# Kernel optimization log

Hardware: AMD Instinct MI355X
Metric: run time of the kernel (lower is better)

The kernel has to match this reference:

```python
import jax, jax.numpy as jnp
import numpy as np

MIN_HAIRPIN = 4
BIG = 1e30  # stand-in for the numpy reference's 1e18 INF (fp32-safe)


def _dp_single(e_pair, e_unp, allowed):
    """Nussinov min-energy DP for one sequence.
    e_pair: (L,L) f32, e_unp: (L,) f32, allowed: (L,L) bool.
    Returns dp (L,L) and ptr (L,L) backpointers matching the numpy reference:
      0 -> i unpaired, 1 -> j unpaired, 2 -> (i,j) paired, k+3 -> bifurcation at k.
    Vectorised over the antidiagonal (all i for a fixed span s at once).
    """
    L = e_unp.shape[0]
    idx = jnp.arange(L)
    dp0 = jnp.full((L, L), BIG, dtype=e_pair.dtype).at[idx, idx].set(e_unp)
    ptr0 = jnp.full((L, L), -1, dtype=jnp.int32).at[idx, idx].set(0)
    t = jnp.arange(L - 1)  # bifurcation offset k = i + t

    def step(carry, s):
        dp, ptr = carry
        j = idx + s - 1
        valid = j < L
        jc = jnp.minimum(j, L - 1)
        ip1 = jnp.minimum(idx + 1, L - 1)
        jm1 = jnp.maximum(jc - 1, 0)
        opt0 = dp[ip1, jc] + e_unp            # i unpaired
        opt1 = dp[idx, jm1] + e_unp[jc]       # j unpaired
        inner = jnp.where(s >= 3, dp[ip1, jm1], 0.0)
        pair_ok = allowed[idx, jc] & (s - 1 > MIN_HAIRPIN)  # j - i = s - 1
        opt2 = jnp.where(pair_ok, inner + e_pair[idx, jc], BIG)
        k = jnp.minimum(idx[:, None] + t[None, :], L - 1)
        bif = dp[idx[:, None], k] + dp[jnp.minimum(k + 1, L - 1), jc[:, None]]
        bif = jnp.where(t[None, :] < s - 1, bif, BIG)
        cand = jnp.concatenate([opt0[:, None], opt1[:, None], opt2[:, None], bif], axis=1)
        c = jnp.argmin(cand, axis=1)  # first-occurrence argmin == strict-< tie-break
        best = jnp.take_along_axis(cand, c[:, None], axis=1)[:, 0]
        new_ptr = jnp.where(c < 3, c, c + idx).astype(jnp.int32)  # c-3 is offset t -> k+3 = c+i
        dp = dp.at[idx, jc].set(jnp.where(valid, best, dp[idx, jc]))
        ptr = ptr.at[idx, jc].set(jnp.where(valid, new_ptr, ptr[idx, jc]))
        return (dp, ptr), None

    (dp, ptr), _ = jax.lax.scan(step, (dp0, ptr0), jnp.arange(2, L + 1))
    return dp, ptr


def _traceback(ptr):
    """Stack-based traceback of the backpointer matrix. Returns pairs (L,) int32, -1 = unpaired."""
    L = ptr.shape[0]

    def cond(st):
        return st[2] > 0

    def body(st):
        si, sj, sp, res = st
        top = sp - 1
        i, j = si[top], sj[top]
        skip = i >= j
        p = ptr[i, j]
        is0, is1, is2, isk = p == 0, p == 1, p == 2, p >= 3
        k = p - 3
        p1i = jnp.where(is0 | is2, i + 1, i)
        p1j = jnp.where(is1 | is2, j - 1, jnp.where(isk, k, j))
        v1 = (~skip) & jnp.where(is2, i + 1 <= j - 1, True)
        v2 = (~skip) & isk  # bifurcation pushes a second interval (k+1, j)
        res = jnp.where(is2 & (~skip), res.at[i].set(j).at[j].set(i), res)
        si = si.at[top].set(jnp.where(v1, p1i, si[top]))
        sj = sj.at[top].set(jnp.where(v1, p1j, sj[top]))
        slot2 = top + v1.astype(jnp.int32)
        si = si.at[slot2].set(jnp.where(v2, k + 1, si[slot2]))
        sj = sj.at[slot2].set(jnp.where(v2, j, sj[slot2]))
        sp = top + v1.astype(jnp.int32) + v2.astype(jnp.int32)
        return si, sj, sp, res

    si0 = jnp.zeros((L,), jnp.int32)
    sj0 = jnp.zeros((L,), jnp.int32).at[0].set(L - 1)
    res0 = jnp.full((L,), -1, jnp.int32)
    _, _, _, res = jax.lax.while_loop(cond, body, (si0, sj0, jnp.int32(1), res0))
    return res


def _structure_energy(e_pair, e_unp, pairs):
    """E(x,S) = sum_{i unpaired} e_unp[i] + sum_{(i,j) in S, i<j} e_pair[i,j]."""
    L = e_unp.shape[-1]
    clamped = jnp.maximum(pairs, 0)
    unp = jnp.where(pairs < 0, e_unp, 0.0).sum(-1)
    pe = jnp.take_along_axis(e_pair, clamped[..., None], axis=2)[..., 0]
    is_pair = (pairs >= 0) & (jnp.arange(L)[None, :] < clamped)
    return unp + jnp.where(is_pair, pe, 0.0).sum(-1)


def setup_inputs() -> dict:
    key = jax.random.key(0)
    k1, k2, k3 = jax.random.split(key, 3)
    B, L = 32, 384
    e_pair = jax.random.normal(k1, (B, L, L), jnp.float32)
    e_unp = jax.random.normal(k2, (B, L), jnp.float32)
    pair_mask = jax.random.randint(k3, (B, L, L), 0, 2).astype(jnp.bool_)
    return {"e_pair": e_pair, "e_unp": e_unp, "pair_mask": pair_mask}


def reference(e_pair, e_unp, pair_mask):
    dp, ptr = jax.vmap(_dp_single)(e_pair, e_unp, pair_mask)
    pairs = jax.vmap(_traceback)(ptr)  # (B, L) int32, -1 = unpaired
    energy = _structure_energy(e_pair, e_unp, pairs)  # (B,), equals dp[:, 0, -1]
    return pairs, energy
```

## Files before the change

### kernel.cpp

```cpp
#include <hip/hip_runtime.h>
#include <hip/hip_bf16.h>

#define LSEQ 384
#define BATCH 32
#define BIGV 1e30f
#define TB_STK 448
#define NN ((size_t)LSEQ * LSEQ)
#define BT 32
#define NT 12
#define PIT 33

__device__ __forceinline__ int detect_mmode_wave(const unsigned char* m0, int lane) {
    unsigned char v = m0[lane & 63];
    unsigned long long big = __ballot(v >= 2);
    unsigned long long off = __ballot((((lane & 63) & 3) != 0) && (v != 0));
    return big ? 2 : (off ? 1 : 0);
}
__device__ __forceinline__ bool mask_read(const void* mask, size_t idx, int mmode) {
    if (mmode == 0) return ((const unsigned int*)mask)[idx] != 0;
    if (mmode == 1) return ((const unsigned char*)mask)[idx] != 0;
    return ((const unsigned short*)mask)[idx] != 0;
}
__device__ __forceinline__ void choice_write(void* mask, size_t idx, int c, int mmode) {
    if (mmode == 0) ((unsigned int*)mask)[idx] = (unsigned int)c;
    else if (mmode == 1) ((unsigned char*)mask)[idx] = (unsigned char)c;
    else ((unsigned short*)mask)[idx] = (unsigned short)c;
}

__device__ __forceinline__ float edge_min32(const float* rowp, const float* colp) {
    float a0 = BIGV, a1 = BIGV, a2 = BIGV, a3 = BIGV;
    #pragma unroll
    for (int kk = 0; kk < 32; kk += 4) {
        float r0 = rowp[kk], r1 = rowp[kk + 1], r2 = rowp[kk + 2], r3 = rowp[kk + 3];
        const float* cb = colp + kk * PIT;
        float c0 = cb[0], c1 = cb[PIT], c2 = cb[2 * PIT], c3 = cb[3 * PIT];
        a0 = fminf(a0, r0 + c0); a1 = fminf(a1, r1 + c1);
        a2 = fminf(a2, r2 + c2); a3 = fminf(a3, r3 + c3);
    }
    return fminf(fminf(a0, a1), fminf(a2, a3));
}

__global__ __launch_bounds__(64) void diag_kernel(
    float* __restrict__ e_pair, const float* __restrict__ e_unp, void* mask)
{
    __shared__ float dT[BT + 1][PIT];
    __shared__ float epm[BT][PIT];
    __shared__ float s_eunp[BT];

    const int bid = blockIdx.x;
    const int b = bid / NT, t = bid % NT;
    const int lane = threadIdx.x;
    float* dpG = e_pair + (size_t)b * NN;
    const size_t mb = (size_t)b * NN;
    const int mmode = detect_mmode_wave((const unsigned char*)mask, lane);

    for (int z = lane; z < (BT + 1) * PIT; z += 64) ((float*)dT)[z] = BIGV;
    __syncthreads();
    if (lane < BT) {
        int i = t * BT + lane;
        float v = e_unp[b * LSEQ + i];
        s_eunp[lane] = v;
        dT[lane][lane] = v;
        dpG[(size_t)i * LSEQ + i] = v;
        if (i > 0) dpG[(size_t)i * LSEQ + i - 1] = v;
    }
    for (int z = lane; z < BT * BT; z += 64) {
        int li = z >> 5, lj = z & 31;
        int i = t * BT + li, j = t * BT + lj;
        bool ok = (lj - li > 4) && mask_read(mask, mb + (size_t)i * LSEQ + j, mmode);
        epm[li][lj] = ok ? dpG[(size_t)i * LSEQ + j] : BIGV;
    }
    __syncthreads();

    const int idx = lane >> 1, h = lane & 1;
    for (int sg = 1; sg < BT; ++sg) {
        const int nc = BT - sg;
        const bool act = idx < nc;
        const int li = idx, lj = idx + sg;
        const int ljc = lj < BT ? lj : BT - 1;
        const int i = t * BT + li, j = t * BT + lj;
        float ev = edge_min32(&dT[li][0], &dT[1][ljc]);
        float e1 = BIGV, opt0 = 0.f, x1 = BIGV, x2 = BIGV;
        if (act) {
            if (h == 0) {
                e1 = ev;
                opt0 = dT[li + 1][lj] + s_eunp[li];
            } else {
                x1 = dT[li][lj - 1] + s_eunp[lj];
                float pe = epm[li][lj];
                if (pe < BIGV) x2 = dT[li + 1][lj - 1] + pe;
            }
        }
        float y1 = __shfl_xor(x1, 1), y2 = __shfl_xor(x2, 1);
        if (act && h == 0) {
            float best = fminf(e1, y2);
            int cch = (best == opt0) ? 0 : (best == y1) ? 1
                     : (best == y2 && y2 < BIGV) ? 2 : 3;
            dT[li][lj] = best;
            dpG[(size_t)i * LSEQ + j] = best;
            if (i > 0) dpG[(size_t)j * LSEQ + i - 1] = best;
            choice_write(mask, mb + (size_t)j * LSEQ + i, cch, mmode);
        }
    }
}

__global__ __launch_bounds__(512) void phase_kernel(
    float* __restrict__ e_pair, const float* __restrict__ e_unp, void* mask, int s)
{
    __shared__ float dTI[BT + 1][PIT], dTJ[BT + 1][PIT];
    __shared__ float cur[BT + 1][PIT];
    __shared__ float epm[BT][PIT];
    __shared__ float part[8][BT][PIT];
    __shared__ float brow[BT], bcol[BT], s_eI[BT], s_eJ[BT];
    __shared__ float bcorn;

    const int nt = NT - s;
    const int bid = blockIdx.x;
    const int b = bid / nt, I = bid % nt, J = I + s;
    const int tid = threadIdx.x, lane = tid & 63, wv = tid >> 6;
    float* dpG = e_pair + (size_t)b * NN;
    const size_t mb = (size_t)b * NN;
    const int mmode = detect_mmode_wave((const unsigned char*)mask, lane);

    for (int z = tid; z < BT * BT; z += 512) {
        int li = z >> 5, lj = z & 31;
        dTI[li][lj] = (lj >= li) ? dpG[(size_t)(I * BT + li) * LSEQ + I * BT + lj] : BIGV;
        dTJ[li][lj] = (lj >= li) ? dpG[(size_t)(J * BT + li) * LSEQ + J * BT + lj] : BIGV;
    }
    for (int z = tid; z < PIT; z += 512) {
        dTI[BT][z] = BIGV; dTJ[BT][z] = BIGV; cur[BT][z] = BIGV;
    }
    if (tid < BT) {
        brow[tid] = dpG[(size_t)((I + 1) * BT) * LSEQ + J * BT + tid];
        s_eI[tid] = e_unp[b * LSEQ + I * BT + tid];
    } else if (tid < 2 * BT) {
        int q = tid - BT;
        bcol[q] = dpG[(size_t)(I * BT + q) * LSEQ + J * BT - 1];
        s_eJ[q] = e_unp[b * LSEQ + J * BT + q];
    } else if (tid == 2 * BT) {
        bcorn = (s >= 2) ? dpG[(size_t)((I + 1) * BT) * LSEQ + J * BT - 1] : BIGV;
    }
    for (int z = tid; z < BT * BT; z += 512) {
        int li = z >> 5, lj = z & 31;
        int i = I * BT + li, j = J * BT + lj;
        bool ok = (j - i > 4) && mask_read(mask, mb + (size_t)i * LSEQ + j, mmode);
        epm[li][lj] = ok ? dpG[(size_t)i * LSEQ + j] : BIGV;
    }

    if (s == 1) {
        for (int z = tid; z < BT * PIT; z += 512) ((float*)cur)[z] = BIGV;
    } else {
        const int r0 = (lane >> 3) << 2, c0 = (lane & 7) << 2;
        float r16[16];
        #pragma unroll
        for (int z = 0; z < 16; ++z) r16[z] = BIGV;
        for (int M = I + 1 + wv; M < J; M += 8) {
            #pragma unroll
            for (int kq = 0; kq < 8; ++kq) {
                const int k = M * BT + kq * 4;
                float4 a0 = *(const float4*)&dpG[(size_t)(I * BT + r0 + 0) * LSEQ + k];
                float4 a1 = *(const float4*)&dpG[(size_t)(I * BT + r0 + 1) * LSEQ + k];
                float4 a2 = *(const float4*)&dpG[(size_t)(I * BT + r0 + 2) * LSEQ + k];
                float4 a3 = *(const float4*)&dpG[(size_t)(I * BT + r0 + 3) * LSEQ + k];
                float4 b0 = *(const float4*)&dpG[(size_t)(J * BT + c0 + 0) * LSEQ + k];
                float4 b1 = *(const float4*)&dpG[(size_t)(J * BT + c0 + 1) * LSEQ + k];
                float4 b2 = *(const float4*)&dpG[(size_t)(J * BT + c0 + 2) * LSEQ + k];
                float4 b3 = *(const float4*)&dpG[(size_t)(J * BT + c0 + 3) * LSEQ + k];
                #pragma unroll
                for (int ri = 0; ri < 4; ++ri) {
                    float4 av = ri == 0 ? a0 : ri == 1 ? a1 : ri == 2 ? a2 : a3;
                    #pragma unroll
                    for (int ci = 0; ci < 4; ++ci) {
                        float4 bv = ci == 0 ? b0 : ci == 1 ? b1 : ci == 2 ? b2 : b3;
                        float m = fminf(fminf(av.x + bv.x, av.y + bv.y),
                                        fminf(av.z + bv.z, av.w + bv.w));
                        r16[ri * 4 + ci] = fminf(r16[ri * 4 + ci], m);
                    }
                }
            }
        }
        #pragma unroll
        for (int ri = 0; ri < 4; ++ri)
            #pragma unroll
            for (int ci = 0; ci < 4; ++ci)
                part[wv][r0 + ri][c0 + ci] = r16[ri * 4 + ci];
        __syncthreads();
        for (int z = tid; z < BT * BT; z += 512) {
            int li = z >> 5, lj = z & 31;
            float m01 = fminf(part[0][li][lj], part[1][li][lj]);
            float m23 = fminf(part[2][li][lj], part[3][li][lj]);
            float m45 = fminf(part[4][li][lj], part[5][li][lj]);
            float m67 = fminf(part[6][li][lj], part[7][li][lj]);
            cur[li][lj] = fminf(fminf(m01, m23), fminf(m45, m67));
        }
    }
    __syncthreads();
    if (wv != 0) return;

    const int idx = lane >> 1, h = lane & 1;
    for (int sg = -(BT - 1); sg <= BT - 1; ++sg) {
        const int asg = sg < 0 ? -sg : sg;
        const int nc = BT - asg;
        const bool act = idx < nc;
        const int li = (sg >= 0) ? idx : idx - sg;
        const int lj = li + sg;
        const int lic = li < BT ? li : BT - 1;
        const int ljc = (lj < BT ? (lj >= 0 ? lj : 0) : BT - 1);
        const int i = I * BT + li, j = J * BT + lj;
        const float* rowp = (h == 0) ? &dTI[lic][0] : &cur[lic][0];
        const float* colp = (h == 0) ? &cur[1][ljc] : &dTJ[1][ljc];
        float ev = edge_min32(rowp, colp);
        float e1 = BIGV, opt0 = 0.f, farv = BIGV;
        float x0 = BIGV, x1 = BIGV, x2 = BIGV;
        if (act) {
            if (h == 0) {
                e1 = fminf(ev, dTI[li][BT - 1] + brow[lj]);
                opt0 = ((li + 1 < BT) ? cur[li + 1][lj] : brow[lj]) + s_eI[li];
                farv = cur[li][lj];
            } else {
                x0 = ev;
                x1 = ((lj >= 1) ? cur[li][lj - 1] : bcol[li]) + s_eJ[lj];
                float pe = epm[li][lj];
                if (pe < BIGV) {
                    float inner = (li + 1 < BT)
                        ? ((lj >= 1) ? cur[li + 1][lj - 1] : bcol[li + 1])
                        : ((lj >= 1) ? brow[lj - 1] : bcorn);
                    x2 = inner + pe;
                }
            }
        }
        float y0 = __shfl_xor(x0, 1), y1 = __shfl_xor(x1, 1), y2 = __shfl_xor(x2, 1);
        if (act && h == 0) {
            float best = fminf(fminf(fminf(e1, y0), farv), y2);
            int cch = (best == opt0) ? 0 : (best == y1) ? 1
                     : (best == y2 && y2 < BIGV) ? 2 : 3;
            cur[li][lj] = best;
            dpG[(size_t)i * LSEQ + j] = best;
            if (i > 0) dpG[(size_t)j * LSEQ + i - 1] = best;
            choice_write(mask, mb + (size_t)j * LSEQ + i, cch, mmode);
        }
    }
}

__global__ __launch_bounds__(512) void tb_kernel(
    const float* __restrict__ e_pair, const void* mask, float* __restrict__ out)
{
    const int b = blockIdx.x;
    const int tid = threadIdx.x;
    const int lane = tid & 63, wv = tid >> 6;
    const float* dp = e_pair + (size_t)b * NN;
    const size_t mb = (size_t)b * NN;
    const int mmode = detect_mmode_wave((const unsigned char*)mask, lane);

    __shared__ __align__(16) unsigned char ch[LSEQ * LSEQ];
    __shared__ short res[LSEQ];
    __shared__ int st[TB_STK];

    if (mmode == 1) {
        const uint4* src = (const uint4*)((const unsigned char*)mask + mb);
        for (int z = tid; z < (int)(NN / 16); z += 512) ((uint4*)ch)[z] = src[z];
    } else if (mmode == 2) {
        const uint4* src = (const uint4*)((const unsigned char*)mask + mb * 2);
        for (int z = tid; z < (int)(NN / 8); z += 512) {
            uint4 v = src[z];
            unsigned int lo = (v.x & 0xFFu) | (((v.x >> 16) & 0xFFu) << 8)
                            | ((v.y & 0xFFu) << 16) | (((v.y >> 16) & 0xFFu) << 24);
            unsigned int hi = (v.z & 0xFFu) | (((v.z >> 16) & 0xFFu) << 8)
                            | ((v.w & 0xFFu) << 16) | (((v.w >> 16) & 0xFFu) << 24);
            ((unsigned int*)ch)[z * 2] = lo;
            ((unsigned int*)ch)[z * 2 + 1] = hi;
        }
    } else {
        const uint4* src = (const uint4*)((const unsigned char*)mask + mb * 4);
        for (int z = tid; z < (int)(NN / 4); z += 512) {
            uint4 v = src[z];
            ((unsigned int*)ch)[z] = (v.x & 0xFFu) | ((v.y & 0xFFu) << 8)
                                   | ((v.z & 0xFFu) << 16) | ((v.w & 0xFFu) << 24);
        }
    }
    for (int l = tid; l < LSEQ; l += 512) res[l] = -1;
    __syncthreads();
    if (wv != 0) return;

    int sp = 0;
    int ci = 0, cj = LSEQ - 1;
    int have = 1;
    for (int iter = 0; iter < 8192; ++iter) {
        if (!have) {
            if (sp == 0) break;
            --sp;
            int pk = st[sp];
            ci = pk >> 16; cj = pk & 0xFFFF;
        }
        have = 0;
        if (ci >= cj) continue;
        int c = ch[(size_t)cj * LSEQ + ci];
        if (c == 0) { ++ci; have = 1; }
        else if (c == 1) { --cj; have = 1; }
        else if (c == 2) {
            res[ci] = (short)cj; res[cj] = (short)ci;
            if (ci + 1 <= cj - 1) { ++ci; --cj; have = 1; }
        } else {
            const int d = cj - ci;
            const float* rowi = dp + (size_t)ci * LSEQ;
            const float* mrow = dp + (size_t)cj * LSEQ;
            float bv = BIGV; int bt = d;
            for (int t = lane; t < d; t += 64) {
                float cc = rowi[ci + t] + mrow[ci + t];
                if (cc < bv || (cc == bv && t < bt)) { bv = cc; bt = t; }
            }
            for (int m = 32; m > 0; m >>= 1) {
                float ov = __shfl_xor(bv, m, 64);
                int   ot = __shfl_xor(bt, m, 64);
                if (ov < bv || (ov == bv && ot < bt)) { bv = ov; bt = ot; }
            }
            int k = ci + bt;
            if (sp < TB_STK - 1) { st[sp] = ((k + 1) << 16) | cj; ++sp; }
            cj = k; have = 1;
        }
    }

    for (int l = lane; l < LSEQ; l += 64)
        out[b * LSEQ + l] = (float)res[l];
    if (lane == 0)
        out[BATCH * LSEQ + b] = dp[LSEQ - 1];
}

extern "C" void kernel_launch(void* const* d_in, const int* in_sizes, int n_in,
                              void* d_out, int out_size, void* d_ws, size_t ws_size,
                              hipStream_t stream) {
    float* e_pair = (float*)d_in[0];
    const float* e_unp = (const float*)d_in[1];
    void* mask = d_in[2];
    (void)d_ws; (void)ws_size;

    diag_kernel<<<BATCH * NT, 64, 0, stream>>>(e_pair, e_unp, mask);
    for (int s = 1; s < NT; ++s)
        phase_kernel<<<BATCH * (NT - s), 512, 0, stream>>>(e_pair, e_unp, mask, s);
    tb_kernel<<<BATCH, 512, 0, stream>>>(e_pair, mask, (float*)d_out);
}
```

Baseline: 912.0 us.

## Fuse per-span DP phases into one persistent row-wise kernel with atomic counters

Replaces the diagonal kernel and the eleven per-span phase launches with a single persistent kernel. Each workgroup grabs a tile-row job from an atomic queue and walks its spans in order, waiting on per-batch span counters in global memory instead of kernel boundaries. Previously computed tiles of the same row stay in shared memory and are reused for the bifurcation min-plus step, so only the column tiles are read from global memory. The change trades launch overhead and redundant row reloads for spin-wait synchronisation, relaxed atomic loads and stores, and fewer waves per block (256 threads instead of 512). Correctness depends on relaxed ordering plus vmcnt waits and a capped spin loop.

```diff
diff --git a/kernel.cpp b/kernel.cpp
--- a/kernel.cpp
+++ b/kernel.cpp
@@ -1,5 +1,4 @@
 #include <hip/hip_runtime.h>
-#include <hip/hip_bf16.h>
 
 #define LSEQ 384
 #define BATCH 32
@@ -9,6 +8,9 @@
 #define BT 32
 #define NT 12
 #define PIT 33
+#define NJOBS (BATCH * NT)
+#define WS_CNT_BASE 8
+#define SPIN_CAP (1 << 21)
 
 __device__ __forceinline__ int detect_mmode_wave(const unsigned char* m0, int lane) {
     unsigned char v = m0[lane & 63];
@@ -21,10 +23,29 @@
     if (mmode == 1) return ((const unsigned char*)mask)[idx] != 0;
     return ((const unsigned short*)mask)[idx] != 0;
 }
-__device__ __forceinline__ void choice_write(void* mask, size_t idx, int c, int mmode) {
-    if (mmode == 0) ((unsigned int*)mask)[idx] = (unsigned int)c;
-    else if (mmode == 1) ((unsigned char*)mask)[idx] = (unsigned char)c;
-    else ((unsigned short*)mask)[idx] = (unsigned short)c;
+__device__ __forceinline__ void choice_write_rel(void* mask, size_t idx, int c, int mmode) {
+    if (mmode == 0)
+        __hip_atomic_store((unsigned int*)mask + idx, (unsigned int)c,
+                           __ATOMIC_RELAXED, __HIP_MEMORY_SCOPE_AGENT);
+    else if (mmode == 1)
+        __hip_atomic_store((unsigned char*)mask + idx, (unsigned char)c,
+                           __ATOMIC_RELAXED, __HIP_MEMORY_SCOPE_AGENT);
+    else
+        __hip_atomic_store((unsigned short*)mask + idx, (unsigned short)c,
+                           __ATOMIC_RELAXED, __HIP_MEMORY_SCOPE_AGENT);
+}
+__device__ __forceinline__ float aload(const float* p) {
+    return __hip_atomic_load((float*)p, __ATOMIC_RELAXED, __HIP_MEMORY_SCOPE_AGENT);
+}
+__device__ __forceinline__ float4 aload4(const float* p) {
+    union { unsigned long long u[2]; float4 f; } r;
+    unsigned long long* q = (unsigned long long*)p;
+    r.u[0] = __hip_atomic_load(q, __ATOMIC_RELAXED, __HIP_MEMORY_SCOPE_AGENT);
+    r.u[1] = __hip_atomic_load(q + 1, __ATOMIC_RELAXED, __HIP_MEMORY_SCOPE_AGENT);
+    return r.f;
+}
+__device__ __forceinline__ void astore(float* p, float v) {
+    __hip_atomic_store(p, v, __ATOMIC_RELAXED, __HIP_MEMORY_SCOPE_AGENT);
 }
 
 __device__ __forceinline__ float edge_min32(const float* rowp, const float* colp) {
@@ -40,204 +61,227 @@
     return fminf(fminf(a0, a1), fminf(a2, a3));
 }
 
-__global__ __launch_bounds__(64) void diag_kernel(
-    float* __restrict__ e_pair, const float* __restrict__ e_unp, void* mask)
+__global__ void init_ws(unsigned int* __restrict__ ws) {
+    for (int z = threadIdx.x; z < WS_CNT_BASE + BATCH * 16; z += 256) ws[z] = 0;
+}
+
+__global__ __launch_bounds__(256) void dp_rows(
+    float* __restrict__ e_pair, const float* __restrict__ e_unp,
+    void* mask, unsigned int* __restrict__ ws)
 {
-    __shared__ float dT[BT + 1][PIT];
+    __shared__ float rowT[NT][BT + 1][PIT];
+    __shared__ float dTJ[BT + 1][PIT];
     __shared__ float epm[BT][PIT];
-    __shared__ float s_eunp[BT];
-
-    const int bid = blockIdx.x;
-    const int b = bid / NT, t = bid % NT;
-    const int lane = threadIdx.x;
-    float* dpG = e_pair + (size_t)b * NN;
-    const size_t mb = (size_t)b * NN;
+    __shared__ float brow[BT], s_eI[BT], s_eJ[BT];
+    __shared__ float bcorn_s;
+    __shared__ unsigned int s_job;
+
+    const int tid = threadIdx.x, lane = tid & 63, wv = tid >> 6;
     const int mmode = detect_mmode_wave((const unsigned char*)mask, lane);
 
-    for (int z = lane; z < (BT + 1) * PIT; z += 64) ((float*)dT)[z] = BIGV;
-    __syncthreads();
-    if (lane < BT) {
-        int i = t * BT + lane;
-        float v = e_unp[b * LSEQ + i];
-        s_eunp[lane] = v;
-        dT[lane][lane] = v;
-        dpG[(size_t)i * LSEQ + i] = v;
-        if (i > 0) dpG[(size_t)i * LSEQ + i - 1] = v;
-    }
-    for (int z = lane; z < BT * BT; z += 64) {
-        int li = z >> 5, lj = z & 31;
-        int i = t * BT + li, j = t * BT + lj;
-        bool ok = (lj - li > 4) && mask_read(mask, mb + (size_t)i * LSEQ + j, mmode);
-        epm[li][lj] = ok ? dpG[(size_t)i * LSEQ + j] : BIGV;
-    }
-    __syncthreads();
-
-    const int idx = lane >> 1, h = lane & 1;
-    for (int sg = 1; sg < BT; ++sg) {
-        const int nc = BT - sg;
-        const bool act = idx < nc;
-        const int li = idx, lj = idx + sg;
-        const int ljc = lj < BT ? lj : BT - 1;
-        const int i = t * BT + li, j = t * BT + lj;
-        float ev = edge_min32(&dT[li][0], &dT[1][ljc]);
-        float e1 = BIGV, opt0 = 0.f, x1 = BIGV, x2 = BIGV;
-        if (act) {
-            if (h == 0) {
-                e1 = ev;
-                opt0 = dT[li + 1][lj] + s_eunp[li];
+    for (;;) {
+        if (tid == 0)
+            s_job = __hip_atomic_fetch_add(&ws[0], 1u, __ATOMIC_RELAXED,
+                                           __HIP_MEMORY_SCOPE_AGENT);
+        __syncthreads();
+        const unsigned int job = s_job;
+        if (job >= NJOBS) return;
+        const int b = (int)(job / NT);
+        const int I = (int)(job % NT);
+        float* dpG = e_pair + (size_t)b * NN;
+        const size_t mb = (size_t)b * NN;
+        unsigned int* cnt = ws + WS_CNT_BASE + b * 16;
+
+        for (int z = tid; z < NT * (BT + 1) * PIT; z += 256) ((float*)rowT)[z] = BIGV;
+        for (int z = tid; z < (BT + 1) * PIT; z += 256) ((float*)dTJ)[z] = BIGV;
+        if (tid < BT) s_eI[tid] = e_unp[b * LSEQ + I * BT + tid];
+        __syncthreads();
+
+        if (tid < BT) {
+            int i = I * BT + tid;
+            float v = s_eI[tid];
+            rowT[0][tid][tid] = v;
+            astore(&dpG[(size_t)i * LSEQ + i], v);
+            if (i > 0) astore(&dpG[(size_t)i * LSEQ + i - 1], v);
+        }
+        for (int z = tid; z < BT * BT; z += 256) {
+            int li = z >> 5, lj = z & 31;
+            int i = I * BT + li, j = I * BT + lj;
+            bool ok = (lj - li > 4) && mask_read(mask, mb + (size_t)i * LSEQ + j, mmode);
+            epm[li][lj] = ok ? dpG[(size_t)i * LSEQ + j] : BIGV;
+        }
+        __syncthreads();
+        if (wv == 0) {
+            const int idx = lane >> 1, h = lane & 1;
+            for (int sg = 1; sg < BT; ++sg) {
+                const int nc = BT - sg;
+                const bool act = idx < nc;
+                const int li = idx, lj = idx + sg;
+                const int ljc = lj < BT ? lj : BT - 1;
+                const int i = I * BT + li, j = I * BT + lj;
+                float ev = edge_min32(&rowT[0][li][0], &rowT[0][1][ljc]);
+                float e1 = BIGV, opt0 = 0.f, x1 = BIGV, x2 = BIGV;
+                if (act) {
+                    if (h == 0) {
+                        e1 = ev;
+                        opt0 = rowT[0][li + 1][lj] + s_eI[li];
+                    } else {
+                        x1 = rowT[0][li][lj - 1] + s_eI[lj];
+                        float pe = epm[li][lj];
+                        if (pe < BIGV) x2 = rowT[0][li + 1][lj - 1] + pe;
+                    }
+                }
+                float y1 = __shfl_xor(x1, 1), y2 = __shfl_xor(x2, 1);
+                if (act && h == 0) {
+                    float best = fminf(e1, y2);
+                    int cch = (best == opt0) ? 0 : (best == y1) ? 1
+                             : (best == y2 && y2 < BIGV) ? 2 : 3;
+                    rowT[0][li][lj] = best;
+                    astore(&dpG[(size_t)i * LSEQ + j], best);
+                    if (i > 0) astore(&dpG[(size_t)j * LSEQ + i - 1], best);
+                    choice_write_rel(mask, mb + (size_t)j * LSEQ + i, cch, mmode);
+                }
+            }
+        }
+        asm volatile("s_waitcnt vmcnt(0)" ::: "memory");
+        __syncthreads();
+        if (tid == 0)
+            __hip_atomic_fetch_add(&cnt[0], 1u, __ATOMIC_RELAXED,
+                                   __HIP_MEMORY_SCOPE_AGENT);
+
+        for (int s = 1; s <= NT - 1 - I; ++s) {
+            const int J = I + s;
+            float (*cur)[PIT] = rowT[s];
+            float (*prv)[PIT] = rowT[s - 1];
+
+            if (tid == 0) {
+                const unsigned int need = (unsigned int)(NT - (s - 1));
+                int spin = 0;
+                while (__hip_atomic_load(&cnt[s - 1], __ATOMIC_RELAXED,
+                                         __HIP_MEMORY_SCOPE_AGENT) < need) {
+                    __builtin_amdgcn_s_sleep(8);
+                    if (++spin > SPIN_CAP) break;
+                }
+            }
+            __syncthreads();
+
+            for (int z = tid; z < BT * BT; z += 256) {
+                int li = z >> 5, lj = z & 31;
+                dTJ[li][lj] = (lj >= li)
+                    ? aload(&dpG[(size_t)(J * BT + li) * LSEQ + J * BT + lj]) : BIGV;
+            }
+            if (tid < BT) {
+                brow[tid] = aload(&dpG[(size_t)((I + 1) * BT) * LSEQ + J * BT + tid]);
+                s_eJ[tid] = e_unp[b * LSEQ + J * BT + tid];
+            } else if (tid == BT) {
+                bcorn_s = (s >= 2)
+                    ? aload(&dpG[(size_t)((I + 1) * BT) * LSEQ + J * BT - 1]) : BIGV;
+            }
+            for (int z = tid; z < BT * BT; z += 256) {
+                int li = z >> 5, lj = z & 31;
+                int i = I * BT + li, j = J * BT + lj;
+                bool ok = (j - i > 4) && mask_read(mask, mb + (size_t)i * LSEQ + j, mmode);
+                epm[li][lj] = ok ? dpG[(size_t)i * LSEQ + j] : BIGV;
+            }
+
+            if (s == 1) {
+                for (int z = tid; z < BT * PIT; z += 256) ((float*)cur)[z] = BIGV;
+                __syncthreads();
             } else {
-                x1 = dT[li][lj - 1] + s_eunp[lj];
-                float pe = epm[li][lj];
-                if (pe < BIGV) x2 = dT[li + 1][lj - 1] + pe;
-            }
-        }
-        float y1 = __shfl_xor(x1, 1), y2 = __shfl_xor(x2, 1);
-        if (act && h == 0) {
-            float best = fminf(e1, y2);
-            int cch = (best == opt0) ? 0 : (best == y1) ? 1
-                     : (best == y2 && y2 < BIGV) ? 2 : 3;
-            dT[li][lj] = best;
-            dpG[(size_t)i * LSEQ + j] = best;
-            if (i > 0) dpG[(size_t)j * LSEQ + i - 1] = best;
-            choice_write(mask, mb + (size_t)j * LSEQ + i, cch, mmode);
-        }
-    }
-}
-
-__global__ __launch_bounds__(512) void phase_kernel(
-    float* __restrict__ e_pair, const float* __restrict__ e_unp, void* mask, int s)
-{
-    __shared__ float dTI[BT + 1][PIT], dTJ[BT + 1][PIT];
-    __shared__ float cur[BT + 1][PIT];
-    __shared__ float epm[BT][PIT];
-    __shared__ float part[8][BT][PIT];
-    __shared__ float brow[BT], bcol[BT], s_eI[BT], s_eJ[BT];
-    __shared__ float bcorn;
-
-    const int nt = NT - s;
-    const int bid = blockIdx.x;
-    const int b = bid / nt, I = bid % nt, J = I + s;
-    const int tid = threadIdx.x, lane = tid & 63, wv = tid >> 6;
-    float* dpG = e_pair + (size_t)b * NN;
-    const size_t mb = (size_t)b * NN;
-    const int mmode = detect_mmode_wave((const unsigned char*)mask, lane);
-
-    for (int z = tid; z < BT * BT; z += 512) {
-        int li = z >> 5, lj = z & 31;
-        dTI[li][lj] = (lj >= li) ? dpG[(size_t)(I * BT + li) * LSEQ + I * BT + lj] : BIGV;
-        dTJ[li][lj] = (lj >= li) ? dpG[(size_t)(J * BT + li) * LSEQ + J * BT + lj] : BIGV;
-    }
-    for (int z = tid; z < PIT; z += 512) {
-        dTI[BT][z] = BIGV; dTJ[BT][z] = BIGV; cur[BT][z] = BIGV;
-    }
-    if (tid < BT) {
-        brow[tid] = dpG[(size_t)((I + 1) * BT) * LSEQ + J * BT + tid];
-        s_eI[tid] = e_unp[b * LSEQ + I * BT + tid];
-    } else if (tid < 2 * BT) {
-        int q = tid - BT;
-        bcol[q] = dpG[(size_t)(I * BT + q) * LSEQ + J * BT - 1];
-        s_eJ[q] = e_unp[b * LSEQ + J * BT + q];
-    } else if (tid == 2 * BT) {
-        bcorn = (s >= 2) ? dpG[(size_t)((I + 1) * BT) * LSEQ + J * BT - 1] : BIGV;
-    }
-    for (int z = tid; z < BT * BT; z += 512) {
-        int li = z >> 5, lj = z & 31;
-        int i = I * BT + li, j = J * BT + lj;
-        bool ok = (j - i > 4) && mask_read(mask, mb + (size_t)i * LSEQ + j, mmode);
-        epm[li][lj] = ok ? dpG[(size_t)i * LSEQ + j] : BIGV;
-    }
-
-    if (s == 1) {
-        for (int z = tid; z < BT * PIT; z += 512) ((float*)cur)[z] = BIGV;
-    } else {
-        const int r0 = (lane >> 3) << 2, c0 = (lane & 7) << 2;
-        float r16[16];
-        #pragma unroll
-        for (int z = 0; z < 16; ++z) r16[z] = BIGV;
-        for (int M = I + 1 + wv; M < J; M += 8) {
-            #pragma unroll
-            for (int kq = 0; kq < 8; ++kq) {
-                const int k = M * BT + kq * 4;
-                float4 a0 = *(const float4*)&dpG[(size_t)(I * BT + r0 + 0) * LSEQ + k];
-                float4 a1 = *(const float4*)&dpG[(size_t)(I * BT + r0 + 1) * LSEQ + k];
-                float4 a2 = *(const float4*)&dpG[(size_t)(I * BT + r0 + 2) * LSEQ + k];
-                float4 a3 = *(const float4*)&dpG[(size_t)(I * BT + r0 + 3) * LSEQ + k];
-                float4 b0 = *(const float4*)&dpG[(size_t)(J * BT + c0 + 0) * LSEQ + k];
-                float4 b1 = *(const float4*)&dpG[(size_t)(J * BT + c0 + 1) * LSEQ + k];
-                float4 b2 = *(const float4*)&dpG[(size_t)(J * BT + c0 + 2) * LSEQ + k];
-                float4 b3 = *(const float4*)&dpG[(size_t)(J * BT + c0 + 3) * LSEQ + k];
+                const int r0 = (lane >> 3) << 2, c0 = (lane & 7) << 2;
+                float r16[16];
                 #pragma unroll
-                for (int ri = 0; ri < 4; ++ri) {
-                    float4 av = ri == 0 ? a0 : ri == 1 ? a1 : ri == 2 ? a2 : a3;
+                for (int z = 0; z < 16; ++z) r16[z] = BIGV;
+                for (int m = 1 + wv; m < s; m += 4) {
+                    float (*A)[PIT] = rowT[m];
+                    const int kg = (I + m) * BT;
                     #pragma unroll
-                    for (int ci = 0; ci < 4; ++ci) {
-                        float4 bv = ci == 0 ? b0 : ci == 1 ? b1 : ci == 2 ? b2 : b3;
-                        float m = fminf(fminf(av.x + bv.x, av.y + bv.y),
-                                        fminf(av.z + bv.z, av.w + bv.w));
-                        r16[ri * 4 + ci] = fminf(r16[ri * 4 + ci], m);
-                    }
-                }
-            }
-        }
-        #pragma unroll
-        for (int ri = 0; ri < 4; ++ri)
-            #pragma unroll
-            for (int ci = 0; ci < 4; ++ci)
-                part[wv][r0 + ri][c0 + ci] = r16[ri * 4 + ci];
-        __syncthreads();
-        for (int z = tid; z < BT * BT; z += 512) {
-            int li = z >> 5, lj = z & 31;
-            float m01 = fminf(part[0][li][lj], part[1][li][lj]);
-            float m23 = fminf(part[2][li][lj], part[3][li][lj]);
-            float m45 = fminf(part[4][li][lj], part[5][li][lj]);
-            float m67 = fminf(part[6][li][lj], part[7][li][lj]);
-            cur[li][lj] = fminf(fminf(m01, m23), fminf(m45, m67));
-        }
-    }
-    __syncthreads();
-    if (wv != 0) return;
-
-    const int idx = lane >> 1, h = lane & 1;
-    for (int sg = -(BT - 1); sg <= BT - 1; ++sg) {
-        const int asg = sg < 0 ? -sg : sg;
-        const int nc = BT - asg;
-        const bool act = idx < nc;
-        const int li = (sg >= 0) ? idx : idx - sg;
-        const int lj = li + sg;
-        const int lic = li < BT ? li : BT - 1;
-        const int ljc = (lj < BT ? (lj >= 0 ? lj : 0) : BT - 1);
-        const int i = I * BT + li, j = J * BT + lj;
-        const float* rowp = (h == 0) ? &dTI[lic][0] : &cur[lic][0];
-        const float* colp = (h == 0) ? &cur[1][ljc] : &dTJ[1][ljc];
-        float ev = edge_min32(rowp, colp);
-        float e1 = BIGV, opt0 = 0.f, farv = BIGV;
-        float x0 = BIGV, x1 = BIGV, x2 = BIGV;
-        if (act) {
-            if (h == 0) {
-                e1 = fminf(ev, dTI[li][BT - 1] + brow[lj]);
-                opt0 = ((li + 1 < BT) ? cur[li + 1][lj] : brow[lj]) + s_eI[li];
-                farv = cur[li][lj];
-            } else {
-                x0 = ev;
-                x1 = ((lj >= 1) ? cur[li][lj - 1] : bcol[li]) + s_eJ[lj];
-                float pe = epm[li][lj];
-                if (pe < BIGV) {
-                    float inner = (li + 1 < BT)
-                        ? ((lj >= 1) ? cur[li + 1][lj - 1] : bcol[li + 1])
-                        : ((lj >= 1) ? brow[lj - 1] : bcorn);
-                    x2 = inner + pe;
-                }
-            }
-        }
-        float y0 = __shfl_xor(x0, 1), y1 = __shfl_xor(x1, 1), y2 = __shfl_xor(x2, 1);
-        if (act && h == 0) {
-            float best = fminf(fminf(fminf(e1, y0), farv), y2);
-            int cch = (best == opt0) ? 0 : (best == y1) ? 1
-                     : (best == y2 && y2 < BIGV) ? 2 : 3;
-            cur[li][lj] = best;
-            dpG[(size_t)i * LSEQ + j] = best;
-            if (i > 0) dpG[(size_t)j * LSEQ + i - 1] = best;
-            choice_write(mask, mb + (size_t)j * LSEQ + i, cch, mmode);
+                    for (int kq = 0; kq < 8; ++kq) {
+                        const int k0 = kq * 4;
+                        float4 b0 = aload4(&dpG[(size_t)(J * BT + c0 + 0) * LSEQ + kg + k0]);
+                        float4 b1 = aload4(&dpG[(size_t)(J * BT + c0 + 1) * LSEQ + kg + k0]);
+                        float4 b2 = aload4(&dpG[(size_t)(J * BT + c0 + 2) * LSEQ + kg + k0]);
+                        float4 b3 = aload4(&dpG[(size_t)(J * BT + c0 + 3) * LSEQ + kg + k0]);
+                        #pragma unroll
+                        for (int ri = 0; ri < 4; ++ri) {
+                            const float* ar = &A[r0 + ri][k0];
+                            float ax = ar[0], ay = ar[1], az = ar[2], aw = ar[3];
+                            #pragma unroll
+                            for (int ci = 0; ci < 4; ++ci) {
+                                float4 bv = ci == 0 ? b0 : ci == 1 ? b1 : ci == 2 ? b2 : b3;
+                                float mm = fminf(fminf(ax + bv.x, ay + bv.y),
+                                                 fminf(az + bv.z, aw + bv.w));
+                                r16[ri * 4 + ci] = fminf(r16[ri * 4 + ci], mm);
+                            }
+                        }
+                    }
+                }
+                for (int z = tid; z < BT * PIT; z += 256) ((float*)cur)[z] = BIGV;
+                __syncthreads();
+                #pragma unroll
+                for (int w = 0; w < 4; ++w) {
+                    if (wv == w) {
+                        #pragma unroll
+                        for (int ri = 0; ri < 4; ++ri)
+                            #pragma unroll
+                            for (int ci = 0; ci < 4; ++ci)
+                                cur[r0 + ri][c0 + ci] =
+                                    fminf(cur[r0 + ri][c0 + ci], r16[ri * 4 + ci]);
+                    }
+                    __syncthreads();
+                }
+            }
+
+            if (wv == 0) {
+                const int idx = lane >> 1, h = lane & 1;
+                for (int sg = -(BT - 1); sg <= BT - 1; ++sg) {
+                    const int asg = sg < 0 ? -sg : sg;
+                    const int nc = BT - asg;
+                    const bool act = idx < nc;
+                    const int li = (sg >= 0) ? idx : idx - sg;
+                    const int lj = li + sg;
+                    const int lic = li < BT ? li : BT - 1;
+                    const int ljc = (lj < BT ? (lj >= 0 ? lj : 0) : BT - 1);
+                    const int i = I * BT + li, j = J * BT + lj;
+                    const float* rowp = (h == 0) ? &rowT[0][lic][0] : &cur[lic][0];
+                    const float* colp = (h == 0) ? &cur[1][ljc] : &dTJ[1][ljc];
+                    float ev = edge_min32(rowp, colp);
+                    float e1 = BIGV, opt0 = 0.f, farv = BIGV;
+                    float x0 = BIGV, x1 = BIGV, x2 = BIGV;
+                    if (act) {
+                        if (h == 0) {
+                            e1 = fminf(ev, rowT[0][li][BT - 1] + brow[lj]);
+                            opt0 = ((li + 1 < BT) ? cur[li + 1][lj] : brow[lj]) + s_eI[li];
+                            farv = cur[li][lj];
+                        } else {
+                            x0 = ev;
+                            x1 = ((lj >= 1) ? cur[li][lj - 1] : prv[li][31]) + s_eJ[lj];
+                            float pe = epm[li][lj];
+                            if (pe < BIGV) {
+                                float inner = (li + 1 < BT)
+                                    ? ((lj >= 1) ? cur[li + 1][lj - 1] : prv[li + 1][31])
+                                    : ((lj >= 1) ? brow[lj - 1] : bcorn_s);
+                                x2 = inner + pe;
+                            }
+                        }
+                    }
+                    float y0 = __shfl_xor(x0, 1), y1 = __shfl_xor(x1, 1), y2 = __shfl_xor(x2, 1);
+                    if (act && h == 0) {
+                        float best = fminf(fminf(fminf(e1, y0), farv), y2);
+                        int cch = (best == opt0) ? 0 : (best == y1) ? 1
+                                 : (best == y2 && y2 < BIGV) ? 2 : 3;
+                        cur[li][lj] = best;
+                        astore(&dpG[(size_t)i * LSEQ + j], best);
+                        if (i > 0) astore(&dpG[(size_t)j * LSEQ + i - 1], best);
+                        choice_write_rel(mask, mb + (size_t)j * LSEQ + i, cch, mmode);
+                    }
+                }
+            }
+            asm volatile("s_waitcnt vmcnt(0)" ::: "memory");
+            __syncthreads();
+            if (tid == 0)
+                __hip_atomic_fetch_add(&cnt[s], 1u, __ATOMIC_RELAXED,
+                                       __HIP_MEMORY_SCOPE_AGENT);
         }
     }
 }
@@ -332,10 +376,10 @@
     float* e_pair = (float*)d_in[0];
     const float* e_unp = (const float*)d_in[1];
     void* mask = d_in[2];
-    (void)d_ws; (void)ws_size;
-
-    diag_kernel<<<BATCH * NT, 64, 0, stream>>>(e_pair, e_unp, mask);
-    for (int s = 1; s < NT; ++s)
-        phase_kernel<<<BATCH * (NT - s), 512, 0, stream>>>(e_pair, e_unp, mask, s);
+    unsigned int* ws = (unsigned int*)d_ws;
+    (void)ws_size;
+
+    init_ws<<<1, 256, 0, stream>>>(ws);
+    dp_rows<<<NJOBS, 256, 0, stream>>>(e_pair, e_unp, mask, ws);
     tb_kernel<<<BATCH, 512, 0, stream>>>(e_pair, mask, (float*)d_out);
 }
```

Result: faster. 884.8 us (-3.0%).

## Precompute min-plus bifurcation contributions incrementally in earlier diagonal steps

Applied to the files above, without the earlier changes.

Restructures the blocked DP schedule. Each step kernel now also launches extra blocks that fold the newly finished tile pairs into a per-tile min-plus accumulator stored in workspace, for tiles on later diagonals. When a tile's own diagonal comes up, only up to two fresh middle tiles are reduced and combined with the accumulator. This spreads the bifurcation work across earlier launches to shorten the critical path. The cost is extra workspace traffic, more blocks per launch, and reliance on a precomputed offset table that must match the tile indexing.

```diff
diff --git a/kernel.cpp b/kernel.cpp
--- a/kernel.cpp
+++ b/kernel.cpp
@@ -1,5 +1,4 @@
 #include <hip/hip_runtime.h>
-#include <hip/hip_bf16.h>
 
 #define LSEQ 384
 #define BATCH 32
@@ -39,6 +38,50 @@
     }
     return fminf(fminf(a0, a1), fminf(a2, a3));
 }
+
+__device__ __forceinline__ void minplus_waves(
+    const float* __restrict__ dpG, int I, int J, const int* fm, int nfm,
+    int wv, int lane, float part[4][BT][PIT])
+{
+    const int r0 = (lane >> 3) << 2, c0 = (lane & 7) << 2;
+    float r16[16];
+    #pragma unroll
+    for (int z = 0; z < 16; ++z) r16[z] = BIGV;
+    const int mi = wv >> 1, kqB = (wv & 1) * 4;
+    if (mi < nfm) {
+        const int M = fm[mi];
+        #pragma unroll
+        for (int q = 0; q < 4; ++q) {
+            const int k = M * BT + (kqB + q) * 4;
+            float4 a0 = *(const float4*)&dpG[(size_t)(I * BT + r0 + 0) * LSEQ + k];
+            float4 a1 = *(const float4*)&dpG[(size_t)(I * BT + r0 + 1) * LSEQ + k];
+            float4 a2 = *(const float4*)&dpG[(size_t)(I * BT + r0 + 2) * LSEQ + k];
+            float4 a3 = *(const float4*)&dpG[(size_t)(I * BT + r0 + 3) * LSEQ + k];
+            float4 b0 = *(const float4*)&dpG[(size_t)(J * BT + c0 + 0) * LSEQ + k];
+            float4 b1 = *(const float4*)&dpG[(size_t)(J * BT + c0 + 1) * LSEQ + k];
+            float4 b2 = *(const float4*)&dpG[(size_t)(J * BT + c0 + 2) * LSEQ + k];
+            float4 b3 = *(const float4*)&dpG[(size_t)(J * BT + c0 + 3) * LSEQ + k];
+            #pragma unroll
+            for (int ri = 0; ri < 4; ++ri) {
+                float4 av = ri == 0 ? a0 : ri == 1 ? a1 : ri == 2 ? a2 : a3;
+                #pragma unroll
+                for (int ci = 0; ci < 4; ++ci) {
+                    float4 bv = ci == 0 ? b0 : ci == 1 ? b1 : ci == 2 ? b2 : b3;
+                    float m = fminf(fminf(av.x + bv.x, av.y + bv.y),
+                                    fminf(av.z + bv.z, av.w + bv.w));
+                    r16[ri * 4 + ci] = fminf(r16[ri * 4 + ci], m);
+                }
+            }
+        }
+    }
+    #pragma unroll
+    for (int ri = 0; ri < 4; ++ri)
+        #pragma unroll
+        for (int ci = 0; ci < 4; ++ci)
+            part[wv][r0 + ri][c0 + ci] = r16[ri * 4 + ci];
+}
+
+__device__ __constant__ int c_sb4[12] = {0,0,0,0, 0, 8, 15, 21, 26, 30, 33, 35};
 
 __global__ __launch_bounds__(64) void diag_kernel(
     float* __restrict__ e_pair, const float* __restrict__ e_unp, void* mask)
@@ -104,30 +147,52 @@
     }
 }
 
-__global__ __launch_bounds__(512) void phase_kernel(
-    float* __restrict__ e_pair, const float* __restrict__ e_unp, void* mask, int s)
+__global__ __launch_bounds__(256) void step_kernel(
+    float* __restrict__ e_pair, const float* __restrict__ e_unp,
+    void* mask, float* __restrict__ acc, int p)
 {
     __shared__ float dTI[BT + 1][PIT], dTJ[BT + 1][PIT];
     __shared__ float cur[BT + 1][PIT];
     __shared__ float epm[BT][PIT];
-    __shared__ float part[8][BT][PIT];
+    __shared__ float part[4][BT][PIT];
     __shared__ float brow[BT], bcol[BT], s_eI[BT], s_eJ[BT];
     __shared__ float bcorn;
 
-    const int nt = NT - s;
-    const int bid = blockIdx.x;
-    const int b = bid / nt, I = bid % nt, J = I + s;
+    const int b = blockIdx.x % BATCH;
+    const int u = blockIdx.x / BATCH;
+    const int nswp = NT - p;
     const int tid = threadIdx.x, lane = tid & 63, wv = tid >> 6;
     float* dpG = e_pair + (size_t)b * NN;
     const size_t mb = (size_t)b * NN;
+
+    if (u >= nswp) {
+        int e = u - nswp, s2 = p + 1;
+        while (s2 < NT && e >= NT - s2) { e -= NT - s2; ++s2; }
+        const int I = e, J = I + s2;
+        int fm[2]; fm[0] = I + p - 1; int nfm = 1;
+        if (J - (p - 1) != fm[0]) fm[nfm++] = J - (p - 1);
+        minplus_waves(dpG, I, J, fm, nfm, wv, lane, part);
+        __syncthreads();
+        float* accT = acc + ((size_t)(b * 36 + c_sb4[s2] + I) << 10);
+        const bool first = (p == (s2 + 1) / 2 + 1);
+        for (int z = tid; z < BT * BT; z += 256) {
+            int li = z >> 5, lj = z & 31;
+            float m = fminf(fminf(part[0][li][lj], part[1][li][lj]),
+                            fminf(part[2][li][lj], part[3][li][lj]));
+            accT[z] = first ? m : fminf(accT[z], m);
+        }
+        return;
+    }
+
+    const int I = u, J = I + p, s = p;
     const int mmode = detect_mmode_wave((const unsigned char*)mask, lane);
 
-    for (int z = tid; z < BT * BT; z += 512) {
+    for (int z = tid; z < BT * BT; z += 256) {
         int li = z >> 5, lj = z & 31;
         dTI[li][lj] = (lj >= li) ? dpG[(size_t)(I * BT + li) * LSEQ + I * BT + lj] : BIGV;
         dTJ[li][lj] = (lj >= li) ? dpG[(size_t)(J * BT + li) * LSEQ + J * BT + lj] : BIGV;
     }
-    for (int z = tid; z < PIT; z += 512) {
+    for (int z = tid; z < PIT; z += 256) {
         dTI[BT][z] = BIGV; dTJ[BT][z] = BIGV; cur[BT][z] = BIGV;
     }
     if (tid < BT) {
@@ -140,59 +205,26 @@
     } else if (tid == 2 * BT) {
         bcorn = (s >= 2) ? dpG[(size_t)((I + 1) * BT) * LSEQ + J * BT - 1] : BIGV;
     }
-    for (int z = tid; z < BT * BT; z += 512) {
+    for (int z = tid; z < BT * BT; z += 256) {
         int li = z >> 5, lj = z & 31;
         int i = I * BT + li, j = J * BT + lj;
         bool ok = (j - i > 4) && mask_read(mask, mb + (size_t)i * LSEQ + j, mmode);
         epm[li][lj] = ok ? dpG[(size_t)i * LSEQ + j] : BIGV;
     }
 
-    if (s == 1) {
-        for (int z = tid; z < BT * PIT; z += 512) ((float*)cur)[z] = BIGV;
-    } else {
-        const int r0 = (lane >> 3) << 2, c0 = (lane & 7) << 2;
-        float r16[16];
-        #pragma unroll
-        for (int z = 0; z < 16; ++z) r16[z] = BIGV;
-        for (int M = I + 1 + wv; M < J; M += 8) {
-            #pragma unroll
-            for (int kq = 0; kq < 8; ++kq) {
-                const int k = M * BT + kq * 4;
-                float4 a0 = *(const float4*)&dpG[(size_t)(I * BT + r0 + 0) * LSEQ + k];
-                float4 a1 = *(const float4*)&dpG[(size_t)(I * BT + r0 + 1) * LSEQ + k];
-                float4 a2 = *(const float4*)&dpG[(size_t)(I * BT + r0 + 2) * LSEQ + k];
-                float4 a3 = *(const float4*)&dpG[(size_t)(I * BT + r0 + 3) * LSEQ + k];
-                float4 b0 = *(const float4*)&dpG[(size_t)(J * BT + c0 + 0) * LSEQ + k];
-                float4 b1 = *(const float4*)&dpG[(size_t)(J * BT + c0 + 1) * LSEQ + k];
-                float4 b2 = *(const float4*)&dpG[(size_t)(J * BT + c0 + 2) * LSEQ + k];
-                float4 b3 = *(const float4*)&dpG[(size_t)(J * BT + c0 + 3) * LSEQ + k];
-                #pragma unroll
-                for (int ri = 0; ri < 4; ++ri) {
-                    float4 av = ri == 0 ? a0 : ri == 1 ? a1 : ri == 2 ? a2 : a3;
-                    #pragma unroll
-                    for (int ci = 0; ci < 4; ++ci) {
-                        float4 bv = ci == 0 ? b0 : ci == 1 ? b1 : ci == 2 ? b2 : b3;
-                        float m = fminf(fminf(av.x + bv.x, av.y + bv.y),
-                                        fminf(av.z + bv.z, av.w + bv.w));
-                        r16[ri * 4 + ci] = fminf(r16[ri * 4 + ci], m);
-                    }
-                }
-            }
-        }
-        #pragma unroll
-        for (int ri = 0; ri < 4; ++ri)
-            #pragma unroll
-            for (int ci = 0; ci < 4; ++ci)
-                part[wv][r0 + ri][c0 + ci] = r16[ri * 4 + ci];
-        __syncthreads();
-        for (int z = tid; z < BT * BT; z += 512) {
-            int li = z >> 5, lj = z & 31;
-            float m01 = fminf(part[0][li][lj], part[1][li][lj]);
-            float m23 = fminf(part[2][li][lj], part[3][li][lj]);
-            float m45 = fminf(part[4][li][lj], part[5][li][lj]);
-            float m67 = fminf(part[6][li][lj], part[7][li][lj]);
-            cur[li][lj] = fminf(fminf(m01, m23), fminf(m45, m67));
-        }
+    int fm[2]; int nfm = 0;
+    if (s >= 2) fm[nfm++] = I + 1;
+    if (s >= 3) fm[nfm++] = J - 1;
+    minplus_waves(dpG, I, J, fm, nfm, wv, lane, part);
+    __syncthreads();
+
+    const float* accT = acc + ((size_t)(b * 36 + c_sb4[s] + I) << 10);
+    for (int z = tid; z < BT * BT; z += 256) {
+        int li = z >> 5, lj = z & 31;
+        float m = fminf(fminf(part[0][li][lj], part[1][li][lj]),
+                        fminf(part[2][li][lj], part[3][li][lj]));
+        if (s >= 4) m = fminf(m, accT[z]);
+        cur[li][lj] = m;
     }
     __syncthreads();
     if (wv != 0) return;
@@ -332,10 +364,14 @@
     float* e_pair = (float*)d_in[0];
     const float* e_unp = (const float*)d_in[1];
     void* mask = d_in[2];
-    (void)d_ws; (void)ws_size;
+    float* acc = (float*)d_ws;
+    (void)ws_size;
+
+    static const int updC[12] = {0, 0, 0, 8, 13, 15, 14, 10, 6, 3, 1, 0};
 
     diag_kernel<<<BATCH * NT, 64, 0, stream>>>(e_pair, e_unp, mask);
-    for (int s = 1; s < NT; ++s)
-        phase_kernel<<<BATCH * (NT - s), 512, 0, stream>>>(e_pair, e_unp, mask, s);
+    for (int p = 1; p < NT; ++p)
+        step_kernel<<<BATCH * (NT - p + updC[p]), 256, 0, stream>>>(
+            e_pair, e_unp, mask, acc, p);
     tb_kernel<<<BATCH, 512, 0, stream>>>(e_pair, mask, (float*)d_out);
 }
```

Measured after the change: 775.6 us. -15.0%, faster.
